# Optimization experiments

Hardware: AMD Instinct MI355X
Metric: run time of the kernel (lower is better)

Reference implementation:

```python
import jax, jax.numpy as jnp
import numpy as np

VEC = 64
HEADS = 16
DUP = 4
HIDDEN = VEC * HEADS * DUP  # 4096
EPS = 1e-12


def setup_inputs() -> dict:
    key = jax.random.key(0)
    ks = jax.random.split(key, 7)
    B, S, N = 4, 512, 512
    out_len = VEC * HEADS
    return {
        "embeddings": jax.random.normal(ks[0], (B, S, HIDDEN), jnp.float32),
        "keys": jax.random.normal(ks[1], (B, N, out_len), jnp.float32),
        "values": jax.random.normal(ks[2], (B, N, out_len), jnp.float32),
        "Wq": jax.random.normal(ks[3], (HIDDEN, HIDDEN), jnp.float32) * (1.0 / np.sqrt(HIDDEN)),
        "bq": jnp.zeros((HIDDEN,), jnp.float32),
        "Wre": jax.random.normal(ks[4], (HIDDEN, HIDDEN), jnp.float32) * (1.0 / np.sqrt(HIDDEN)),
        "bre": jnp.zeros((HIDDEN,), jnp.float32),
        "ln_g": jnp.ones((HIDDEN,), jnp.float32),
        "ln_b": jnp.zeros((HIDDEN,), jnp.float32),
    }


def reference(embeddings, keys, values, Wq, bq, Wre, bre, ln_g, ln_b):
    B, S, _ = embeddings.shape
    N = keys.shape[1]
    # query projection: (B,S,hidden) -> reshape to (B, S*DUP, VEC, HEADS) -> (B,H,S*DUP,VEC)
    q = embeddings @ Wq.T + bq
    q = q.reshape(B, S * DUP, VEC, HEADS).transpose(0, 3, 1, 2)
    # keys: (B,N,VEC*HEADS) -> (B,H,VEC,N); values -> (B,H,N,VEC)
    k = keys.reshape(B, N, VEC, HEADS).transpose(0, 3, 2, 1)
    v = values.reshape(B, N, VEC, HEADS).transpose(0, 3, 1, 2)
    scores = jnp.matmul(q, k) / np.sqrt(VEC).astype(np.float32)  # (B,H,S*DUP,N)
    probs = jax.nn.softmax(scores, axis=-1)
    out = jnp.matmul(probs, v)  # (B,H,S*DUP,VEC)
    # (B,H,S*DUP,VEC) -> (B,H,S,VEC*DUP) -> (B,S,H,VEC*DUP) -> (B,S,HIDDEN)
    out = out.reshape(B, HEADS, S, VEC * DUP).transpose(0, 2, 1, 3).reshape(B, S, HIDDEN)
    # LayerNorm (biased variance, torch semantics)
    mu = jnp.mean(out, axis=-1, keepdims=True)
    var = jnp.mean(jnp.square(out - mu), axis=-1, keepdims=True)
    ln = (out - mu) / jnp.sqrt(var + EPS) * ln_g + ln_b
    return ln @ Wre.T + bre
```

## Files before the change

kernel.cpp:

```cpp
#include <hip/hip_runtime.h>

typedef unsigned short u16;
typedef unsigned int   u32;
typedef __attribute__((ext_vector_type(8))) _Float16 half8;
typedef __attribute__((ext_vector_type(4))) _Float16 half4;
typedef __attribute__((ext_vector_type(4))) float    floatx4;

#define GLD16(g, l)                                                            \
  __builtin_amdgcn_global_load_lds(                                            \
      (const __attribute__((address_space(1))) void*)(g),                      \
      (__attribute__((address_space(3))) void*)(l), 16, 0, 0)

__global__ __launch_bounds__(256) void cvt_f16(const float* __restrict__ in,
                                               _Float16* __restrict__ out,
                                               int n8) {
  int i = blockIdx.x * 256 + threadIdx.x;
  if (i >= n8) return;
  const float4* p = (const float4*)in + (size_t)i * 2;
  float4 a = p[0], b = p[1];
  half8 h;
  h[0] = (_Float16)a.x; h[1] = (_Float16)a.y; h[2] = (_Float16)a.z; h[3] = (_Float16)a.w;
  h[4] = (_Float16)b.x; h[5] = (_Float16)b.y; h[6] = (_Float16)b.z; h[7] = (_Float16)b.w;
  *(half8*)(out + (size_t)i * 8) = h;
}

__global__ __launch_bounds__(256) void prep_kv(const float* __restrict__ keys,
                                               const float* __restrict__ values,
                                               _Float16* __restrict__ Kh,
                                               _Float16* __restrict__ Vt) {
  int tid = blockIdx.x * 256 + threadIdx.x;
  {
    int v = tid & 63, n = (tid >> 6) & 511, h = (tid >> 15) & 15, b = tid >> 19;
    Kh[tid] = (_Float16)keys[((size_t)(b * 512 + n)) * 1024 + v * 16 + h];
  }
  {
    int n = tid & 511, v = (tid >> 9) & 63, h = (tid >> 15) & 15, b = tid >> 19;
    Vt[tid] = (_Float16)values[((size_t)(b * 512 + n)) * 1024 + v * 16 + h];
  }
}

template <int MODE>
__global__ __launch_bounds__(256) void gemm_bt(const _Float16* __restrict__ A,
                                               const _Float16* __restrict__ Bw,
                                               const float* __restrict__ bias,
                                               float* __restrict__ Cf,
                                               _Float16* __restrict__ Cb) {
  const int N = 4096, K = 4096;
  __shared__ _Float16 lA[128 * 32];
  __shared__ _Float16 lB[128 * 32];
  const int t = threadIdx.x;
  const int lane = t & 63;
  const int w = t >> 6;
  const int m0 = blockIdx.y * 128, n0 = blockIdx.x * 128;
  const int wm = (w >> 1) * 64, wn = (w & 1) * 64;
  const int fr = lane & 15, fq = lane >> 4;

  floatx4 acc[4][4];
#pragma unroll
  for (int i = 0; i < 4; i++)
#pragma unroll
    for (int j = 0; j < 4; j++) acc[i][j] = (floatx4)(0.f);

  const int r0 = t >> 2, kc0 = (t & 3) * 8;
  const _Float16* gA = A + (size_t)(m0 + r0) * K + kc0;
  const _Float16* gB = Bw + (size_t)(n0 + r0) * K + kc0;
  _Float16* dA = &lA[t * 8];
  _Float16* dB = &lB[t * 8];

  for (int k0 = 0; k0 < K; k0 += 32) {
    GLD16(gA, dA);
    GLD16(gA + (size_t)64 * K, dA + 2048);
    GLD16(gB, dB);
    GLD16(gB + (size_t)64 * K, dB + 2048);
    gA += 32;
    gB += 32;
    __syncthreads();
    half8 af[4], bf[4];
#pragma unroll
    for (int i = 0; i < 4; i++)
      af[i] = *(const half8*)&lA[(wm + i * 16 + fr) * 32 + fq * 8];
#pragma unroll
    for (int j = 0; j < 4; j++)
      bf[j] = *(const half8*)&lB[(wn + j * 16 + fr) * 32 + fq * 8];
#pragma unroll
    for (int i = 0; i < 4; i++)
#pragma unroll
      for (int j = 0; j < 4; j++)
        acc[i][j] =
            __builtin_amdgcn_mfma_f32_16x16x32_f16(af[i], bf[j], acc[i][j], 0, 0, 0);
    __syncthreads();
  }

#pragma unroll
  for (int i = 0; i < 4; i++) {
#pragma unroll
    for (int j = 0; j < 4; j++) {
      const int col = n0 + wn + j * 16 + fr;
      const float bv = bias[col];
      const int rbase = m0 + wm + i * 16 + fq * 4;
      if (MODE == 0) {
#pragma unroll
        for (int r = 0; r < 4; r++)
          Cf[(size_t)(rbase + r) * N + col] = acc[i][j][r] + bv;
      } else {
        const int d = col >> 10, v = (col >> 4) & 63, h = col & 15;
#pragma unroll
        for (int r = 0; r < 4; r++) {
          const int row = rbase + r;
          const int b = row >> 9, s = row & 511;
          Cb[(((size_t)(b * 16 + h) * 2048) + (s * 4 + d)) * 64 + v] =
              (_Float16)((acc[i][j][r] + bv) * 0.125f);
        }
      }
    }
  }
}

__global__ __launch_bounds__(256) void attn_mfma(const _Float16* __restrict__ Q,
                                                 const _Float16* __restrict__ Kh,
                                                 const _Float16* __restrict__ Vt,
                                                 float* __restrict__ Out) {
  __shared__ _Float16 Pbuf[4][32][136];
  const int t = threadIdx.x, lane = t & 63, w = t >> 6;
  const int fr = lane & 15, fq = lane >> 4;
  const int bh = blockIdx.y, qt = blockIdx.x;
  const int b = bh >> 4, h = bh & 15;

  const _Float16* Qb = Q + ((size_t)bh * 2048 + qt * 128 + w * 32) * 64;
  const _Float16* Kb = Kh + (size_t)bh * 512 * 64;
  const _Float16* Vb = Vt + (size_t)bh * 64 * 512;

  half8 qf[2][2];
#pragma unroll
  for (int i = 0; i < 2; i++)
#pragma unroll
    for (int ks = 0; ks < 2; ks++)
      qf[i][ks] = *(const half8*)(Qb + (i * 16 + fr) * 64 + ks * 32 + fq * 8);

  floatx4 oacc[2][4];
  float l_acc[2][4];
#pragma unroll
  for (int i = 0; i < 2; i++)
#pragma unroll
    for (int j = 0; j < 4; j++) {
      oacc[i][j] = (floatx4)(0.f);
      l_acc[i][j] = 0.f;
    }

  for (int c0 = 0; c0 < 512; c0 += 128) {
    floatx4 sc[2][8];
#pragma unroll
    for (int i = 0; i < 2; i++)
#pragma unroll
      for (int j = 0; j < 8; j++) sc[i][j] = (floatx4)(0.f);
#pragma unroll
    for (int j = 0; j < 8; j++) {
      const _Float16* kr = Kb + (size_t)(c0 + j * 16 + fr) * 64 + fq * 8;
      half8 k0 = *(const half8*)kr;
      half8 k1 = *(const half8*)(kr + 32);
#pragma unroll
      for (int i = 0; i < 2; i++) {
        sc[i][j] = __builtin_amdgcn_mfma_f32_16x16x32_f16(qf[i][0], k0, sc[i][j], 0, 0, 0);
        sc[i][j] = __builtin_amdgcn_mfma_f32_16x16x32_f16(qf[i][1], k1, sc[i][j], 0, 0, 0);
      }
    }
#pragma unroll
    for (int i = 0; i < 2; i++)
#pragma unroll
      for (int j = 0; j < 8; j++)
#pragma unroll
        for (int r = 0; r < 4; r++) {
          float p = __expf(sc[i][j][r]);
          l_acc[i][r] += p;
          Pbuf[w][i * 16 + fq * 4 + r][j * 16 + fr] = (_Float16)p;
        }
#pragma unroll
    for (int kn = 0; kn < 4; kn++) {
      half8 pa[2];
#pragma unroll
      for (int i = 0; i < 2; i++)
        pa[i] = *(const half8*)&Pbuf[w][i * 16 + fr][kn * 32 + fq * 8];
#pragma unroll
      for (int jv = 0; jv < 4; jv++) {
        half8 vb = *(const half8*)(Vb + (size_t)(jv * 16 + fr) * 512 + c0 + kn * 32 + fq * 8);
#pragma unroll
        for (int i = 0; i < 2; i++)
          oacc[i][jv] = __builtin_amdgcn_mfma_f32_16x16x32_f16(pa[i], vb, oacc[i][jv], 0, 0, 0);
      }
    }
  }

#pragma unroll
  for (int i = 0; i < 2; i++)
#pragma unroll
    for (int r = 0; r < 4; r++) {
#pragma unroll
      for (int m = 8; m; m >>= 1)
        l_acc[i][r] += __shfl_xor(l_acc[i][r], m, 16);
    }
#pragma unroll
  for (int i = 0; i < 2; i++) {
#pragma unroll
    for (int r = 0; r < 4; r++) {
      const float inv = 1.f / l_acc[i][r];
      const int m2 = qt * 128 + w * 32 + i * 16 + fq * 4 + r;
      float* orow = Out + ((size_t)(b * 512 + (m2 >> 2))) * 4096 + h * 256 + (m2 & 3) * 64 + fr;
#pragma unroll
      for (int jv = 0; jv < 4; jv++) orow[jv * 16] = oacc[i][jv][r] * inv;
    }
  }
}

__global__ __launch_bounds__(256) void ln_kernel(const float* __restrict__ X,
                                                 const float* __restrict__ g,
                                                 const float* __restrict__ bb,
                                                 _Float16* __restrict__ Y) {
  const int row = blockIdx.x;
  const int t = threadIdx.x;
  const float* x = X + (size_t)row * 4096;
  float4 vals[4];
  float sum = 0.f, sq = 0.f;
#pragma unroll
  for (int c = 0; c < 4; c++) {
    vals[c] = *(const float4*)&x[c * 1024 + t * 4];
    sum += vals[c].x + vals[c].y + vals[c].z + vals[c].w;
    sq += vals[c].x * vals[c].x + vals[c].y * vals[c].y + vals[c].z * vals[c].z +
          vals[c].w * vals[c].w;
  }
#pragma unroll
  for (int off = 32; off > 0; off >>= 1) {
    sum += __shfl_down(sum, off, 64);
    sq += __shfl_down(sq, off, 64);
  }
  __shared__ float red[8];
  const int w = t >> 6;
  if ((t & 63) == 0) {
    red[w] = sum;
    red[4 + w] = sq;
  }
  __syncthreads();
  sum = red[0] + red[1] + red[2] + red[3];
  sq = red[4] + red[5] + red[6] + red[7];
  const float mu = sum * (1.f / 4096.f);
  float var = sq * (1.f / 4096.f) - mu * mu;
  var = fmaxf(var, 0.f);
  const float rstd = rsqrtf(var + 1e-12f);
#pragma unroll
  for (int c = 0; c < 4; c++) {
    const int j = c * 1024 + t * 4;
    float4 gg = *(const float4*)&g[j];
    float4 bv = *(const float4*)&bb[j];
    half4 y;
    y[0] = (_Float16)((vals[c].x - mu) * rstd * gg.x + bv.x);
    y[1] = (_Float16)((vals[c].y - mu) * rstd * gg.y + bv.y);
    y[2] = (_Float16)((vals[c].z - mu) * rstd * gg.z + bv.z);
    y[3] = (_Float16)((vals[c].w - mu) * rstd * gg.w + bv.w);
    *(half4*)&Y[(size_t)row * 4096 + j] = y;
  }
}

extern "C" void kernel_launch(void* const* d_in, const int* in_sizes, int n_in,
                              void* d_out, int out_size, void* d_ws,
                              size_t ws_size, hipStream_t stream) {
  const float* emb = (const float*)d_in[0];
  const float* keys = (const float*)d_in[1];
  const float* values = (const float*)d_in[2];
  const float* Wq = (const float*)d_in[3];
  const float* bq = (const float*)d_in[4];
  const float* Wre = (const float*)d_in[5];
  const float* bre = (const float*)d_in[6];
  const float* ln_g = (const float*)d_in[7];
  const float* ln_b = (const float*)d_in[8];
  float* out = (float*)d_out;

  char* ws = (char*)d_ws;
  _Float16* embH = (_Float16*)(ws);
  _Float16* WH = (_Float16*)(ws + ((size_t)16 << 20));
  _Float16* qattn = (_Float16*)(ws + ((size_t)48 << 20));
  _Float16* Kh = (_Float16*)(ws);
  _Float16* Vt = (_Float16*)(ws + ((size_t)8 << 20));
  _Float16* lnH = qattn;
  float* attnO = out;

  cvt_f16<<<4096, 256, 0, stream>>>(emb, embH, 8388608 / 8);
  cvt_f16<<<8192, 256, 0, stream>>>(Wq, WH, 16777216 / 8);
  gemm_bt<1><<<dim3(32, 16), 256, 0, stream>>>(embH, WH, bq, nullptr, qattn);
  prep_kv<<<8192, 256, 0, stream>>>(keys, values, Kh, Vt);
  attn_mfma<<<dim3(16, 64), 256, 0, stream>>>(qattn, Kh, Vt, attnO);
  ln_kernel<<<2048, 256, 0, stream>>>(attnO, ln_g, ln_b, lnH);
  cvt_f16<<<8192, 256, 0, stream>>>(Wre, WH, 16777216 / 8);
  gemm_bt<0><<<dim3(32, 16), 256, 0, stream>>>(lnH, WH, bre, out, nullptr);
}
```

Measured before the change: 504.8 us.

## Split-K both GEMMs across two partitions and add LDS read swizzle

Each 2048x4096x4096 GEMM now runs with a z-dimension of two, each half covering 2048 of K, doubling the block count from 512 to 1024 for better CU occupancy on a 256-CU part. Partial sums go to fp16 buffers (and fp32 output for one half), and new combine kernels add the partials plus bias and apply the 0.125 scale. The global-to-LDS column order and the fragment read offset are swizzled so that LDS reads hit fewer bank conflicts. This adds two elementwise passes and extra memory traffic, and rounds partial sums to fp16 before they are combined.

```diff
diff --git a/kernel.cpp b/kernel.cpp
--- a/kernel.cpp
+++ b/kernel.cpp
@@ -42,9 +42,9 @@
 template <int MODE>
 __global__ __launch_bounds__(256) void gemm_bt(const _Float16* __restrict__ A,
                                                const _Float16* __restrict__ Bw,
-                                               const float* __restrict__ bias,
                                                float* __restrict__ Cf,
-                                               _Float16* __restrict__ Cb) {
+                                               _Float16* __restrict__ H0,
+                                               _Float16* __restrict__ H1) {
   const int N = 4096, K = 4096;
   __shared__ _Float16 lA[128 * 32];
   __shared__ _Float16 lB[128 * 32];
@@ -52,6 +52,7 @@
   const int lane = t & 63;
   const int w = t >> 6;
   const int m0 = blockIdx.y * 128, n0 = blockIdx.x * 128;
+  const int kb = blockIdx.z * 2048;
   const int wm = (w >> 1) * 64, wn = (w & 1) * 64;
   const int fr = lane & 15, fq = lane >> 4;
 
@@ -61,13 +62,15 @@
 #pragma unroll
     for (int j = 0; j < 4; j++) acc[i][j] = (floatx4)(0.f);
 
-  const int r0 = t >> 2, kc0 = (t & 3) * 8;
-  const _Float16* gA = A + (size_t)(m0 + r0) * K + kc0;
-  const _Float16* gB = Bw + (size_t)(n0 + r0) * K + kc0;
+  const int r0 = t >> 2;
+  const int kc0 = (((t & 3) - ((t >> 3) & 3)) & 3) * 8;
+  const _Float16* gA = A + (size_t)(m0 + r0) * K + kb + kc0;
+  const _Float16* gB = Bw + (size_t)(n0 + r0) * K + kb + kc0;
   _Float16* dA = &lA[t * 8];
   _Float16* dB = &lB[t * 8];
-
-  for (int k0 = 0; k0 < K; k0 += 32) {
+  const int kof = ((fq + ((fr >> 1) & 3)) & 3) * 8;
+
+  for (int k0 = 0; k0 < 2048; k0 += 32) {
     GLD16(gA, dA);
     GLD16(gA + (size_t)64 * K, dA + 2048);
     GLD16(gB, dB);
@@ -78,10 +81,10 @@
     half8 af[4], bf[4];
 #pragma unroll
     for (int i = 0; i < 4; i++)
-      af[i] = *(const half8*)&lA[(wm + i * 16 + fr) * 32 + fq * 8];
+      af[i] = *(const half8*)&lA[(wm + i * 16 + fr) * 32 + kof];
 #pragma unroll
     for (int j = 0; j < 4; j++)
-      bf[j] = *(const half8*)&lB[(wn + j * 16 + fr) * 32 + fq * 8];
+      bf[j] = *(const half8*)&lB[(wn + j * 16 + fr) * 32 + kof];
 #pragma unroll
     for (int i = 0; i < 4; i++)
 #pragma unroll
@@ -91,29 +94,68 @@
     __syncthreads();
   }
 
+  const int z = blockIdx.z;
 #pragma unroll
   for (int i = 0; i < 4; i++) {
 #pragma unroll
     for (int j = 0; j < 4; j++) {
       const int col = n0 + wn + j * 16 + fr;
-      const float bv = bias[col];
       const int rbase = m0 + wm + i * 16 + fq * 4;
       if (MODE == 0) {
-#pragma unroll
-        for (int r = 0; r < 4; r++)
-          Cf[(size_t)(rbase + r) * N + col] = acc[i][j][r] + bv;
+        if (z == 0) {
+#pragma unroll
+          for (int r = 0; r < 4; r++)
+            Cf[(size_t)(rbase + r) * N + col] = acc[i][j][r];
+        } else {
+#pragma unroll
+          for (int r = 0; r < 4; r++)
+            H1[(size_t)(rbase + r) * N + col] = (_Float16)acc[i][j][r];
+        }
       } else {
+        _Float16* dst = z ? H1 : H0;
         const int d = col >> 10, v = (col >> 4) & 63, h = col & 15;
 #pragma unroll
         for (int r = 0; r < 4; r++) {
           const int row = rbase + r;
           const int b = row >> 9, s = row & 511;
-          Cb[(((size_t)(b * 16 + h) * 2048) + (s * 4 + d)) * 64 + v] =
-              (_Float16)((acc[i][j][r] + bv) * 0.125f);
+          dst[(((size_t)(b * 16 + h) * 2048) + (s * 4 + d)) * 64 + v] =
+              (_Float16)acc[i][j][r];
         }
       }
     }
   }
+}
+
+__global__ __launch_bounds__(256) void combine1(const _Float16* __restrict__ p0,
+                                                const _Float16* __restrict__ p1,
+                                                const float* __restrict__ bq,
+                                                _Float16* __restrict__ q) {
+  const int j8 = (blockIdx.x * 256 + threadIdx.x) * 8;
+  half8 a = *(const half8*)(p0 + j8);
+  half8 b = *(const half8*)(p1 + j8);
+  const int v0 = j8 & 63;
+  const int d = (j8 >> 6) & 3;
+  const int h = (j8 >> 17) & 15;
+  const int colbase = d * 1024 + v0 * 16 + h;
+  half8 o;
+#pragma unroll
+  for (int r = 0; r < 8; r++)
+    o[r] = (_Float16)(((float)a[r] + (float)b[r] + bq[colbase + r * 16]) * 0.125f);
+  *(half8*)(q + j8) = o;
+}
+
+__global__ __launch_bounds__(256) void combine2(float* __restrict__ out,
+                                                const _Float16* __restrict__ p1,
+                                                const float* __restrict__ bre) {
+  const int i4 = (blockIdx.x * 256 + threadIdx.x) * 4;
+  float4 o = *(float4*)&out[i4];
+  half4 p = *(const half4*)(p1 + i4);
+  float4 bb = *(const float4*)&bre[i4 & 4095];
+  o.x += (float)p[0] + bb.x;
+  o.y += (float)p[1] + bb.y;
+  o.z += (float)p[2] + bb.z;
+  o.w += (float)p[3] + bb.w;
+  *(float4*)&out[i4] = o;
 }
 
 __global__ __launch_bounds__(256) void attn_mfma(const _Float16* __restrict__ Q,
@@ -275,19 +317,24 @@
 
   char* ws = (char*)d_ws;
   _Float16* embH = (_Float16*)(ws);
-  _Float16* WH = (_Float16*)(ws + ((size_t)16 << 20));
-  _Float16* qattn = (_Float16*)(ws + ((size_t)48 << 20));
-  _Float16* Kh = (_Float16*)(ws);
-  _Float16* Vt = (_Float16*)(ws + ((size_t)8 << 20));
-  _Float16* lnH = qattn;
-  float* attnO = out;
+  _Float16* WqH = (_Float16*)(ws + ((size_t)16 << 20));
+  _Float16* p1q = (_Float16*)(ws + ((size_t)48 << 20));
+  _Float16* p0q = (_Float16*)d_out;
+  _Float16* qattn = (_Float16*)(ws);
+  _Float16* Kh = (_Float16*)(ws + ((size_t)48 << 20));
+  _Float16* Vt = (_Float16*)(ws + ((size_t)52 << 20));
+  _Float16* lnH = (_Float16*)(ws + ((size_t)16 << 20));
+  _Float16* WreH = (_Float16*)(ws + ((size_t)32 << 20));
+  _Float16* p1o = (_Float16*)(ws);
 
   cvt_f16<<<4096, 256, 0, stream>>>(emb, embH, 8388608 / 8);
-  cvt_f16<<<8192, 256, 0, stream>>>(Wq, WH, 16777216 / 8);
-  gemm_bt<1><<<dim3(32, 16), 256, 0, stream>>>(embH, WH, bq, nullptr, qattn);
+  cvt_f16<<<8192, 256, 0, stream>>>(Wq, WqH, 16777216 / 8);
+  gemm_bt<1><<<dim3(32, 16, 2), 256, 0, stream>>>(embH, WqH, nullptr, p0q, p1q);
+  combine1<<<4096, 256, 0, stream>>>(p0q, p1q, bq, qattn);
   prep_kv<<<8192, 256, 0, stream>>>(keys, values, Kh, Vt);
-  attn_mfma<<<dim3(16, 64), 256, 0, stream>>>(qattn, Kh, Vt, attnO);
-  ln_kernel<<<2048, 256, 0, stream>>>(attnO, ln_g, ln_b, lnH);
-  cvt_f16<<<8192, 256, 0, stream>>>(Wre, WH, 16777216 / 8);
-  gemm_bt<0><<<dim3(32, 16), 256, 0, stream>>>(lnH, WH, bre, out, nullptr);
-}
+  attn_mfma<<<dim3(16, 64), 256, 0, stream>>>(qattn, Kh, Vt, out);
+  ln_kernel<<<2048, 256, 0, stream>>>(out, ln_g, ln_b, lnH);
+  cvt_f16<<<8192, 256, 0, stream>>>(Wre, WreH, 16777216 / 8);
+  gemm_bt<0><<<dim3(32, 16, 2), 256, 0, stream>>>(lnH, WreH, out, nullptr, p1o);
+  combine2<<<8192, 256, 0, stream>>>(out, p1o, bre);
+}
```

Result: slower. 533.2 us (+5.6%).
